# Kernel tuning notes

Measured on AMD Instinct MI355X. Metric: run time of the kernel, lower is better.

Reference implementation:

```python
import jax, jax.numpy as jnp
import numpy as np

SPAN_W = 8      # fixed span width (tokens per span)
HID = 150       # Score hidden dim (hardcoded in source)


def _score_mlp(x, w1, b1, w2, b2, w3, b3):
    # Linear->ReLU->(Dropout=id)->Linear->ReLU->(Dropout=id)->Linear ; out dim 1
    h = jax.nn.relu(x @ w1 + b1)
    h = jax.nn.relu(h @ w2 + b2)
    return h @ w3 + b3


def _make_mlp_params(key, in_dim):
    ks = jax.random.split(key, 6)
    s1 = 1.0 / np.sqrt(in_dim)
    s2 = 1.0 / np.sqrt(HID)
    return (
        jax.random.uniform(ks[0], (in_dim, HID), jnp.float32, -s1, s1),
        jax.random.uniform(ks[1], (HID,), jnp.float32, -s1, s1),
        jax.random.uniform(ks[2], (HID, HID), jnp.float32, -s2, s2),
        jax.random.uniform(ks[3], (HID,), jnp.float32, -s2, s2),
        jax.random.uniform(ks[4], (HID, 1), jnp.float32, -s2, s2),
        jax.random.uniform(ks[5], (1,), jnp.float32, -s2, s2),
    )


def setup_inputs() -> dict:
    key = jax.random.key(0)
    k_emb, k_sp, k_a, k_m, k_p = jax.random.split(key, 5)
    E = 768
    B, T, S = 2, 2048, 96
    encoded_docs = jax.random.normal(k_emb, (B, T, E), jnp.float32)
    span_starts = jnp.sort(
        jax.random.randint(k_sp, (B, S), 0, 2040, dtype=jnp.int64), axis=-1)
    aw1, ab1, aw2, ab2, aw3, ab3 = _make_mlp_params(k_a, E)          # attn Score
    mw1, mb1, mw2, mb2, mw3, mb3 = _make_mlp_params(k_m, 3 * E)      # mention Score
    pw1, pb1, pw2, pb2, pw3, pb3 = _make_mlp_params(k_p, 9 * E)      # pair Score
    return {
        "encoded_docs": encoded_docs, "span_starts": span_starts,
        "aw1": aw1, "ab1": ab1, "aw2": aw2, "ab2": ab2, "aw3": aw3, "ab3": ab3,
        "mw1": mw1, "mb1": mb1, "mw2": mw2, "mb2": mb2, "mw3": mw3, "mb3": mb3,
        "pw1": pw1, "pb1": pb1, "pw2": pw2, "pb2": pb2, "pw3": pw3, "pb3": pb3,
    }


def reference(encoded_docs, span_starts,
              aw1, ab1, aw2, ab2, aw3, ab3,
              mw1, mb1, mw2, mb2, mw3, mb3,
              pw1, pb1, pw2, pb2, pw3, pb3):
    B, T, E = encoded_docs.shape
    S = span_starts.shape[1]

    # --- MentionScore ---
    attns = _score_mlp(encoded_docs, aw1, ab1, aw2, ab2, aw3, ab3)  # [B,T,1]
    starts = span_starts                                              # [B,S]
    ends = starts + (SPAN_W - 1)
    g_start = jnp.take_along_axis(encoded_docs, starts[:, :, None], axis=1)  # [B,S,E]
    g_end = jnp.take_along_axis(encoded_docs, ends[:, :, None], axis=1)      # [B,S,E]
    tok_idx = starts[:, :, None] + jnp.arange(SPAN_W, dtype=starts.dtype)     # [B,S,W]
    flat = tok_idx.reshape(B, S * SPAN_W)
    span_emb = jnp.take_along_axis(encoded_docs, flat[:, :, None], axis=1).reshape(B, S, SPAN_W, E)
    span_attn = jnp.take_along_axis(attns, flat[:, :, None], axis=1).reshape(B, S, SPAN_W, 1)
    g_attn = jnp.sum(span_emb * span_attn, axis=2)                    # [B,S,E]
    g_i = jnp.concatenate([g_start, g_end, g_attn], axis=-1)          # [B,S,3E]
    mention_scores = _score_mlp(g_i, mw1, mb1, mw2, mb2, mw3, mb3)    # [B,S,1]

    # --- PairwiseScore: all pairs (i=span_1, j=span_2) ---
    gi = jnp.broadcast_to(g_i[:, :, None, :], (B, S, S, 3 * E))
    gj = jnp.broadcast_to(g_i[:, None, :, :], (B, S, S, 3 * E))
    pair = jnp.concatenate([gi, gj, gi * gj], axis=-1)                # [B,S,S,9E]
    pair_scores = _score_mlp(pair, pw1, pb1, pw2, pb2, pw3, pb3)      # [B,S,S,1]
    ext = (mention_scores[:, :, None, :] + mention_scores[:, None, :, :] + pair_scores) / 3.0
    return jnp.clip(ext, 0.0, 1.0)
```

## Files before the change

### kernel.cpp

```cpp
#include <hip/hip_runtime.h>

#define EDIM   768
#define E3     2304
#define HIDD   150
#define TT     2048
#define SS     96
#define BB     2

typedef unsigned short u16;
using frag   = __attribute__((ext_vector_type(8))) short;
using f32x4v = __attribute__((ext_vector_type(4))) float;
using u16x8  = __attribute__((ext_vector_type(8))) unsigned short;

__device__ __forceinline__ u16 bf16rn(float f) {
    union { float f; unsigned u; } v; v.f = f;
    unsigned r = v.u + 0x7FFF + ((v.u >> 16) & 1);
    return (u16)(r >> 16);
}
__device__ __forceinline__ float bf16tof(u16 h) {
    union { unsigned u; float f; } v; v.u = ((unsigned)h) << 16;
    return v.f;
}
__device__ __forceinline__ void split2(float f, u16& hi, u16& lo) {
    hi = bf16rn(f); lo = bf16rn(f - bf16tof(hi));
}
__device__ __forceinline__ int swzoff(int row, int qd) {
    return row * 32 + (((qd + (row >> 1)) & 3) << 3);
}
__device__ __forceinline__ void async16(const void* g, void* l) {
    __builtin_amdgcn_global_load_lds(
        (const __attribute__((address_space(1))) void*)g,
        (__attribute__((address_space(3))) void*)l, 16, 0, 0);
}

__global__ __launch_bounds__(256) void k_prep_all(
    const float* __restrict__ pw1, const float* __restrict__ mw1,
    const float* __restrict__ aw1, const float* __restrict__ aw2,
    const float* __restrict__ pw2, const float* __restrict__ mw2,
    u16* __restrict__ W12t_hi, u16* __restrict__ W12t_lo,
    u16* __restrict__ AW1t_hi, u16* __restrict__ AW1t_lo,
    u16* __restrict__ AW2t_hi, u16* __restrict__ AW2t_lo,
    u16* __restrict__ PW2t_hi, u16* __restrict__ PW2t_lo,
    u16* __restrict__ MW2t_hi, u16* __restrict__ MW2t_lo)
{
    __shared__ float tile[64][33];
    const int bi = blockIdx.x;
    const int t  = threadIdx.x;

    if (bi < 720) {
        const int k0 = (bi % 36) * 64;
        const int n0 = (bi / 36) * 32;
        const int seg = n0 / 160;
        const int nloc0 = n0 - seg * 160;
        for (int idx = t; idx < 2048; idx += 256) {
            const int kk = idx >> 5, nn = idx & 31;
            const int nl = nloc0 + nn;
            const int k  = k0 + kk;
            float v = 0.f;
            if (nl < HIDD) {
                if (seg == 0)      v = pw1[(long)k * HIDD + nl];
                else if (seg == 1) v = pw1[(long)(E3 + k) * HIDD + nl];
                else if (seg == 2) v = mw1[(long)k * HIDD + nl];
                else               v = pw1[(long)(2 * E3 + k) * HIDD + nl];
            }
            tile[kk][nn] = v;
        }
        __syncthreads();
        for (int idx = t; idx < 2048; idx += 256) {
            const int nn = idx >> 6, kk = idx & 63;
            u16 hi, lo; split2(tile[kk][nn], hi, lo);
            W12t_hi[(long)(n0 + nn) * E3 + k0 + kk] = hi;
            W12t_lo[(long)(n0 + nn) * E3 + k0 + kk] = lo;
        }
    } else if (bi < 1488) {
        const int k = bi - 720;
        if (t < 160) {
            float v = (t < HIDD) ? aw1[k * HIDD + t] : 0.f;
            u16 hi, lo; split2(v, hi, lo);
            AW1t_hi[(long)t * EDIM + k] = hi;
            AW1t_lo[(long)t * EDIM + k] = lo;
        }
    } else {
        const int r = bi - 1488;
        const int k = r % 160;
        const int which = r / 160;
        const float* src = (which == 0) ? aw2 : (which == 1) ? pw2 : mw2;
        u16* dh = (which == 0) ? AW2t_hi : (which == 1) ? PW2t_hi : MW2t_hi;
        u16* dl = (which == 0) ? AW2t_lo : (which == 1) ? PW2t_lo : MW2t_lo;
        if (t < 160) {
            float v = (t < HIDD && k < HIDD) ? src[k * HIDD + t] : 0.f;
            u16 hi, lo; split2(v, hi, lo);
            dh[t * 160 + k] = hi;
            dl[t * 160 + k] = lo;
        }
    }
}

__global__ __launch_bounds__(256) void k_attn1(
    const float* __restrict__ X, const int* __restrict__ spans,
    const u16* __restrict__ AW1t_hi, const u16* __restrict__ AW1t_lo,
    float* __restrict__ AH1)
{
    __shared__ __align__(16) u16 As_hi[32 * 40];
    __shared__ __align__(16) u16 As_lo[32 * 40];
    __shared__ __align__(16) u16 Bs_hi[160 * 40];
    __shared__ __align__(16) u16 Bs_lo[160 * 40];

    const int t    = threadIdx.x;
    const int lane = t & 63;
    const int m    = lane & 15;
    const int quad = lane >> 4;
    const int w    = t >> 6;
    const int mt   = (w & 1) * 16;
    const int nb   = (w >> 1) * 80;
    const int ks   = blockIdx.y;

    const int rr = t >> 3, q = t & 7;
    const int grow = blockIdx.x * 32 + rr;
    const int bs = grow >> 3, sw = grow & 7;
    const int b  = bs / SS;
    const int tok = spans[bs] + sw;
    const float* arow = X + ((long)b * TT + tok) * EDIM;

    f32x4v acc[5];
    #pragma unroll
    for (int ht = 0; ht < 5; ++ht)
        #pragma unroll
        for (int r = 0; r < 4; ++r) acc[ht][r] = 0.f;

    for (int tt = 0; tt < 6; ++tt) {
        const int kk0 = ks * 192 + tt * 32;
        {
            const float4 xv = *(const float4*)&arow[kk0 + q * 4];
            ushort4 hv, lv;
            split2(xv.x, hv.x, lv.x); split2(xv.y, hv.y, lv.y);
            split2(xv.z, hv.z, lv.z); split2(xv.w, hv.w, lv.w);
            *(ushort4*)&As_hi[rr * 40 + q * 4] = hv;
            *(ushort4*)&As_lo[rr * 40 + q * 4] = lv;
        }
        #pragma unroll
        for (int it = 0; it < 3; ++it) {
            const int v = t + it * 256;
            if (v < 640) {
                const int h = v >> 2, qq = v & 3;
                *(uint4*)&Bs_hi[h * 40 + qq * 8] = *(const uint4*)&AW1t_hi[(long)h * EDIM + kk0 + qq * 8];
                *(uint4*)&Bs_lo[h * 40 + qq * 8] = *(const uint4*)&AW1t_lo[(long)h * EDIM + kk0 + qq * 8];
            }
        }
        __syncthreads();
        const frag ah = *(const frag*)&As_hi[(mt + m) * 40 + quad * 8];
        const frag al = *(const frag*)&As_lo[(mt + m) * 40 + quad * 8];
        #pragma unroll
        for (int ht = 0; ht < 5; ++ht) {
            const frag bh = *(const frag*)&Bs_hi[(nb + ht * 16 + m) * 40 + quad * 8];
            const frag bl = *(const frag*)&Bs_lo[(nb + ht * 16 + m) * 40 + quad * 8];
            acc[ht] = __builtin_amdgcn_mfma_f32_16x16x32_bf16(al, bh, acc[ht], 0, 0, 0);
            acc[ht] = __builtin_amdgcn_mfma_f32_16x16x32_bf16(ah, bl, acc[ht], 0, 0, 0);
            acc[ht] = __builtin_amdgcn_mfma_f32_16x16x32_bf16(ah, bh, acc[ht], 0, 0, 0);
        }
        __syncthreads();
    }
    #pragma unroll
    for (int ht = 0; ht < 5; ++ht) {
        #pragma unroll
        for (int r = 0; r < 4; ++r) {
            const int row = blockIdx.x * 32 + mt + quad * 4 + r;
            const int col = nb + ht * 16 + m;
            if (col < HIDD) atomicAdd(&AH1[row * 160 + col], acc[ht][r]);
        }
    }
}

__global__ __launch_bounds__(256) void k_attn2(
    const float* __restrict__ AH1,
    const u16* __restrict__ AW2t_hi, const u16* __restrict__ AW2t_lo,
    const float* __restrict__ ab1, const float* __restrict__ ab2,
    const float* __restrict__ aw3, const float* __restrict__ ab3,
    float* __restrict__ attn_g)
{
    __shared__ __align__(16) u16 As_hi[32 * 40];
    __shared__ __align__(16) u16 As_lo[32 * 40];
    __shared__ __align__(16) u16 Bs_hi[160 * 40];
    __shared__ __align__(16) u16 Bs_lo[160 * 40];
    __shared__ float h1s[32 * 160];
    __shared__ float red[32];

    const int t    = threadIdx.x;
    const int lane = t & 63;
    const int m    = lane & 15;
    const int quad = lane >> 4;
    const int w    = t >> 6;
    const int mt   = (w & 1) * 16;
    const int nb   = (w >> 1) * 80;

    for (int u = t; u < 1280; u += 256) {
        const int row = u / 40, c4 = u - (u / 40) * 40;
        const int c0 = c4 * 4;
        const float4 v = *(const float4*)&AH1[(blockIdx.x * 32 + row) * 160 + c0];
        h1s[row * 160 + c0 + 0] = (c0 + 0 < HIDD) ? fmaxf(v.x + ab1[c0 + 0], 0.f) : 0.f;
        h1s[row * 160 + c0 + 1] = (c0 + 1 < HIDD) ? fmaxf(v.y + ab1[c0 + 1], 0.f) : 0.f;
        h1s[row * 160 + c0 + 2] = (c0 + 2 < HIDD) ? fmaxf(v.z + ab1[c0 + 2], 0.f) : 0.f;
        h1s[row * 160 + c0 + 3] = (c0 + 3 < HIDD) ? fmaxf(v.w + ab1[c0 + 3], 0.f) : 0.f;
    }
    if (t < 32) red[t] = 0.f;
    __syncthreads();

    const int rr = t >> 3, q = t & 7;
    f32x4v acc2[5];
    #pragma unroll
    for (int ht = 0; ht < 5; ++ht)
        #pragma unroll
        for (int r = 0; r < 4; ++r) acc2[ht][r] = 0.f;

    for (int kk = 0; kk < 5; ++kk) {
        {
            const float4 xv = *(const float4*)&h1s[rr * 160 + kk * 32 + q * 4];
            ushort4 hv, lv;
            split2(xv.x, hv.x, lv.x); split2(xv.y, hv.y, lv.y);
            split2(xv.z, hv.z, lv.z); split2(xv.w, hv.w, lv.w);
            *(ushort4*)&As_hi[rr * 40 + q * 4] = hv;
            *(ushort4*)&As_lo[rr * 40 + q * 4] = lv;
        }
        #pragma unroll
        for (int it = 0; it < 3; ++it) {
            const int v = t + it * 256;
            if (v < 640) {
                const int h = v >> 2, qq = v & 3;
                *(uint4*)&Bs_hi[h * 40 + qq * 8] = *(const uint4*)&AW2t_hi[h * 160 + kk * 32 + qq * 8];
                *(uint4*)&Bs_lo[h * 40 + qq * 8] = *(const uint4*)&AW2t_lo[h * 160 + kk * 32 + qq * 8];
            }
        }
        __syncthreads();
        const frag ah = *(const frag*)&As_hi[(mt + m) * 40 + quad * 8];
        const frag al = *(const frag*)&As_lo[(mt + m) * 40 + quad * 8];
        #pragma unroll
        for (int ht = 0; ht < 5; ++ht) {
            const frag bh = *(const frag*)&Bs_hi[(nb + ht * 16 + m) * 40 + quad * 8];
            const frag bl = *(const frag*)&Bs_lo[(nb + ht * 16 + m) * 40 + quad * 8];
            acc2[ht] = __builtin_amdgcn_mfma_f32_16x16x32_bf16(al, bh, acc2[ht], 0, 0, 0);
            acc2[ht] = __builtin_amdgcn_mfma_f32_16x16x32_bf16(ah, bl, acc2[ht], 0, 0, 0);
            acc2[ht] = __builtin_amdgcn_mfma_f32_16x16x32_bf16(ah, bh, acc2[ht], 0, 0, 0);
        }
        __syncthreads();
    }

    float s[4] = {0.f, 0.f, 0.f, 0.f};
    #pragma unroll
    for (int ht = 0; ht < 5; ++ht) {
        const int col = nb + ht * 16 + m;
        if (col < HIDD) {
            const float w3 = aw3[col];
            #pragma unroll
            for (int r = 0; r < 4; ++r)
                s[r] += fmaxf(acc2[ht][r] + ab2[col], 0.f) * w3;
        }
    }
    #pragma unroll
    for (int r = 0; r < 4; ++r) {
        for (int off = 8; off > 0; off >>= 1) s[r] += __shfl_down(s[r], off, 16);
    }
    if (m == 0) {
        #pragma unroll
        for (int r = 0; r < 4; ++r) atomicAdd(&red[mt + quad * 4 + r], s[r]);
    }
    __syncthreads();
    if (t < 32) attn_g[blockIdx.x * 32 + t] = red[t] + ab3[0];
}

__global__ __launch_bounds__(256) void k_span_g(
    const float* __restrict__ X, const int* __restrict__ spans,
    const float* __restrict__ attn_g, float* __restrict__ G_ws,
    u16* __restrict__ Gs_hi, u16* __restrict__ Gs_lo)
{
    __shared__ float a8[8];
    const int t  = threadIdx.x;
    const int bs = blockIdx.x;
    const int b  = bs / SS;
    const int start = spans[bs];
    const float* xb = X + ((long)b * TT + start) * EDIM;
    float* Gp = G_ws + (long)bs * E3;
    u16* Gh = Gs_hi + (long)bs * E3;
    u16* Gl = Gs_lo + (long)bs * E3;
    if (t < 8) a8[t] = attn_g[bs * 8 + t];
    __syncthreads();

    for (int e = t; e < EDIM; e += 256) {
        const float gs = xb[e];
        const float ge = xb[7 * EDIM + e];
        float ga = 0.f;
        #pragma unroll
        for (int w = 0; w < 8; ++w) ga += xb[w * EDIM + e] * a8[w];
        Gp[e] = gs; Gp[EDIM + e] = ge; Gp[2 * EDIM + e] = ga;
        u16 hi, lo;
        split2(gs, hi, lo); Gh[e] = hi;            Gl[e] = lo;
        split2(ge, hi, lo); Gh[EDIM + e] = hi;     Gl[EDIM + e] = lo;
        split2(ga, hi, lo); Gh[2 * EDIM + e] = hi; Gl[2 * EDIM + e] = lo;
    }
}

__global__ __launch_bounds__(256) void k_uvm(
    const u16* __restrict__ Gs_hi, const u16* __restrict__ Gs_lo,
    const u16* __restrict__ W9t_hi, const u16* __restrict__ W9t_lo,
    float* __restrict__ UVM)
{
    __shared__ __align__(16) u16 As_hi[64 * 40];
    __shared__ __align__(16) u16 As_lo[64 * 40];
    __shared__ __align__(16) u16 Bs_hi[160 * 40];
    __shared__ __align__(16) u16 Bs_lo[160 * 40];

    const int t    = threadIdx.x;
    const int mb   = blockIdx.x;
    const int nb   = blockIdx.y;
    const int ks   = blockIdx.z;
    const int lane = t & 63;
    const int m    = lane & 15;
    const int quad = lane >> 4;
    const int w    = t >> 6;
    const int mhalf = (w & 1) * 32;
    const int nbase = (w >> 1) * 80;
    const int arr = t >> 2, aq = t & 3;

    f32x4v acc[2][5];
    #pragma unroll
    for (int i = 0; i < 2; ++i)
        #pragma unroll
        for (int j = 0; j < 5; ++j)
            #pragma unroll
            for (int r = 0; r < 4; ++r) acc[i][j][r] = 0.f;

    for (int tt = 0; tt < 6; ++tt) {
        const int kk0 = ks * 192 + tt * 32;
        *(uint4*)&As_hi[arr * 40 + aq * 8] = *(const uint4*)&Gs_hi[(long)(mb * 64 + arr) * E3 + kk0 + aq * 8];
        *(uint4*)&As_lo[arr * 40 + aq * 8] = *(const uint4*)&Gs_lo[(long)(mb * 64 + arr) * E3 + kk0 + aq * 8];
        #pragma unroll
        for (int it = 0; it < 3; ++it) {
            const int v = t + it * 256;
            if (v < 640) {
                const int h = v >> 2, qq = v & 3;
                *(uint4*)&Bs_hi[h * 40 + qq * 8] = *(const uint4*)&W9t_hi[(long)(nb * 160 + h) * E3 + kk0 + qq * 8];
                *(uint4*)&Bs_lo[h * 40 + qq * 8] = *(const uint4*)&W9t_lo[(long)(nb * 160 + h) * E3 + kk0 + qq * 8];
            }
        }
        __syncthreads();
        frag ah[2], al[2];
        #pragma unroll
        for (int mt = 0; mt < 2; ++mt) {
            ah[mt] = *(const frag*)&As_hi[(mhalf + mt * 16 + m) * 40 + quad * 8];
            al[mt] = *(const frag*)&As_lo[(mhalf + mt * 16 + m) * 40 + quad * 8];
        }
        #pragma unroll
        for (int ht = 0; ht < 5; ++ht) {
            const frag bh = *(const frag*)&Bs_hi[(nbase + ht * 16 + m) * 40 + quad * 8];
            const frag bl = *(const frag*)&Bs_lo[(nbase + ht * 16 + m) * 40 + quad * 8];
            #pragma unroll
            for (int mt = 0; mt < 2; ++mt) {
                acc[mt][ht] = __builtin_amdgcn_mfma_f32_16x16x32_bf16(al[mt], bh, acc[mt][ht], 0, 0, 0);
                acc[mt][ht] = __builtin_amdgcn_mfma_f32_16x16x32_bf16(ah[mt], bl, acc[mt][ht], 0, 0, 0);
                acc[mt][ht] = __builtin_amdgcn_mfma_f32_16x16x32_bf16(ah[mt], bh, acc[mt][ht], 0, 0, 0);
            }
        }
        __syncthreads();
    }
    float* dst = UVM + (long)nb * (192 * 160);
    #pragma unroll
    for (int mt = 0; mt < 2; ++mt) {
        #pragma unroll
        for (int ht = 0; ht < 5; ++ht) {
            #pragma unroll
            for (int r = 0; r < 4; ++r) {
                const int row = mb * 64 + mhalf + mt * 16 + quad * 4 + r;
                const int c   = nbase + ht * 16 + m;
                atomicAdd(&dst[row * 160 + c], acc[mt][ht][r]);
            }
        }
    }
}

__global__ __launch_bounds__(256) void k_pairmm(
    const float* __restrict__ G_ws,
    const u16* __restrict__ PCt_hi, const u16* __restrict__ PCt_lo,
    float* __restrict__ H1parts)
{
    __shared__ float gis[768];
    __shared__ __align__(16) float gjst[96 * 32];
    __shared__ __align__(16) u16 As_hi[96 * 32];
    __shared__ __align__(16) u16 As_lo[96 * 32];
    __shared__ __align__(16) u16 Bs_hi[160 * 32];
    __shared__ __align__(16) u16 Bs_lo[160 * 32];

    const int t  = threadIdx.x;
    const int ks = blockIdx.x;
    const int i  = blockIdx.y;
    const int b  = blockIdx.z;
    const int ksbase = ks * 768;
    const int jt0 = i >> 4;
    const int ntiles = 6 - jt0;
    const int j0 = jt0 * 16;
    const int R  = 96 - j0;
    const int nI = R >> 3;

    const int lane = t & 63;
    const int m    = lane & 15;
    const int quad = lane >> 4;
    const int w    = t >> 6;
    const int hb   = (w & 1) * 80;
    const int apar = w >> 1;

    const int Bl_h  = lane >> 2;
    const int Bl_c  = lane & 3;
    const int gj_r  = lane >> 3;
    const int gj_c  = lane & 7;

    const float* Gi = G_ws + (long)(b * SS + i) * E3 + ksbase;
    for (int e = t; e < 768; e += 256) gis[e] = Gi[e];

    f32x4v acc[3][5];
    #pragma unroll
    for (int jt = 0; jt < 3; ++jt)
        #pragma unroll
        for (int ht = 0; ht < 5; ++ht)
            #pragma unroll
            for (int r = 0; r < 4; ++r) acc[jt][ht][r] = 0.f;

    for (int tt = 0; tt < 24; ++tt) {
        const int kk0 = ksbase + tt * 32;
        for (int q2 = w; q2 < 10; q2 += 4) {
            const int h  = q2 * 16 + Bl_h;
            const int qd = (Bl_c - (h >> 1)) & 3;
            const long so = (long)h * E3 + kk0 + qd * 8;
            async16(&PCt_hi[so], &Bs_hi[q2 * 512]);
            async16(&PCt_lo[so], &Bs_lo[q2 * 512]);
        }
        for (int g2 = w; g2 < nI; g2 += 4) {
            const int row = j0 + g2 * 8 + gj_r;
            async16(&G_ws[(long)(b * SS + row) * E3 + kk0 + gj_c * 4],
                    &gjst[g2 * 256]);
        }
        __syncthreads();

        for (int u = t; u < R * 4; u += 256) {
            const int rr = u >> 2, qd = u & 3;
            const float4 g0 = *(const float4*)&gjst[rr * 32 + qd * 8];
            const float4 g1 = *(const float4*)&gjst[rr * 32 + qd * 8 + 4];
            const int kl = tt * 32 + qd * 8;
            u16x8 hv, lv; u16 h, l;
            split2(g0.x * gis[kl + 0], h, l); hv[0] = h; lv[0] = l;
            split2(g0.y * gis[kl + 1], h, l); hv[1] = h; lv[1] = l;
            split2(g0.z * gis[kl + 2], h, l); hv[2] = h; lv[2] = l;
            split2(g0.w * gis[kl + 3], h, l); hv[3] = h; lv[3] = l;
            split2(g1.x * gis[kl + 4], h, l); hv[4] = h; lv[4] = l;
            split2(g1.y * gis[kl + 5], h, l); hv[5] = h; lv[5] = l;
            split2(g1.z * gis[kl + 6], h, l); hv[6] = h; lv[6] = l;
            split2(g1.w * gis[kl + 7], h, l); hv[7] = h; lv[7] = l;
            const int o = swzoff(rr, qd);
            *(u16x8*)&As_hi[o] = hv;
            *(u16x8*)&As_lo[o] = lv;
        }
        __syncthreads();

        frag ah[3], al[3];
        #pragma unroll
        for (int u = 0; u < 3; ++u) {
            const int a = apar + 2 * u;
            if (a < ntiles) {
                const int o = swzoff(a * 16 + m, quad);
                ah[u] = *(const frag*)&As_hi[o];
                al[u] = *(const frag*)&As_lo[o];
            }
        }
        #pragma unroll
        for (int ht = 0; ht < 5; ++ht) {
            const int o = swzoff(hb + ht * 16 + m, quad);
            const frag bh = *(const frag*)&Bs_hi[o];
            const frag bl = *(const frag*)&Bs_lo[o];
            #pragma unroll
            for (int u = 0; u < 3; ++u) {
                if (apar + 2 * u < ntiles) {
                    acc[u][ht] = __builtin_amdgcn_mfma_f32_16x16x32_bf16(al[u], bh, acc[u][ht], 0, 0, 0);
                    acc[u][ht] = __builtin_amdgcn_mfma_f32_16x16x32_bf16(ah[u], bl, acc[u][ht], 0, 0, 0);
                    acc[u][ht] = __builtin_amdgcn_mfma_f32_16x16x32_bf16(ah[u], bh, acc[u][ht], 0, 0, 0);
                }
            }
        }
        __syncthreads();
    }

    float* dst = H1parts + (long)ks * ((long)BB * SS * SS * 160);
    #pragma unroll
    for (int u = 0; u < 3; ++u) {
        const int a = apar + 2 * u;
        if (a < ntiles) {
            #pragma unroll
            for (int ht = 0; ht < 5; ++ht) {
                #pragma unroll
                for (int r = 0; r < 4; ++r) {
                    const int j = (jt0 + a) * 16 + quad * 4 + r;
                    const int h = hb + ht * 16 + m;
                    dst[((long)(b * SS + i) * SS + j) * 160 + h] = acc[u][ht][r];
                }
            }
        }
    }
}

__global__ __launch_bounds__(256) void k_pair2(
    const float* __restrict__ H1a, const float* __restrict__ H1b,
    const float* __restrict__ H1c,
    const float* __restrict__ U_ws, const float* __restrict__ V_ws,
    const float* __restrict__ pb1, const float* __restrict__ m_ws,
    const u16* __restrict__ PW2t_hi, const u16* __restrict__ PW2t_lo,
    const float* __restrict__ pb2, const float* __restrict__ pw3,
    const float* __restrict__ pb3,
    float* __restrict__ out)
{
    __shared__ __align__(16) u16 As_hi[96 * 168];
    __shared__ __align__(16) u16 As_lo[96 * 168];
    __shared__ __align__(16) u16 Bs_hi[160 * 40];
    __shared__ __align__(16) u16 Bs_lo[160 * 40];
    __shared__ float uv[160];
    __shared__ float red[96];

    const int t  = threadIdx.x;
    const int bi = blockIdx.x;
    const int b  = bi / SS;
    const int ii = bi - b * SS;

    if (t < 160) uv[t] = U_ws[bi * 160 + t] + ((t < HIDD) ? pb1[t] : 0.f);
    if (t < 96) red[t] = 0.f;
    __syncthreads();

    for (int u = t; u < 96 * 40; u += 256) {
        const int j = u / 40, hq = u - (u / 40) * 40;
        const int h0 = hq * 4;
        const int mn = ii < j ? ii : j;
        const int mx = ii < j ? j : ii;
        const long idx = (((long)b * SS + mn) * SS + mx) * 160 + h0;
        const float4 a  = *(const float4*)&H1a[idx];
        const float4 bb = *(const float4*)&H1b[idx];
        const float4 c  = *(const float4*)&H1c[idx];
        const float4 vv = *(const float4*)&V_ws[(b * SS + j) * 160 + h0];
        const float p0 = fmaxf(a.x + bb.x + c.x + vv.x + uv[h0 + 0], 0.f);
        const float p1 = fmaxf(a.y + bb.y + c.y + vv.y + uv[h0 + 1], 0.f);
        const float p2 = fmaxf(a.z + bb.z + c.z + vv.z + uv[h0 + 2], 0.f);
        const float p3 = fmaxf(a.w + bb.w + c.w + vv.w + uv[h0 + 3], 0.f);
        ushort4 hv, lv;
        split2(p0, hv.x, lv.x); split2(p1, hv.y, lv.y);
        split2(p2, hv.z, lv.z); split2(p3, hv.w, lv.w);
        *(ushort4*)&As_hi[j * 168 + h0] = hv;
        *(ushort4*)&As_lo[j * 168 + h0] = lv;
    }
    __syncthreads();

    const int lane = t & 63;
    const int m    = lane & 15;
    const int quad = lane >> 4;
    const int w    = t >> 6;
    const int jbs  = (w & 1) * 48;
    const int nbs  = (w >> 1) * 80;

    f32x4v acc[3][5];
    #pragma unroll
    for (int jt = 0; jt < 3; ++jt)
        #pragma unroll
        for (int ht = 0; ht < 5; ++ht)
            #pragma unroll
            for (int r = 0; r < 4; ++r) acc[jt][ht][r] = 0.f;

    for (int kk = 0; kk < 5; ++kk) {
        #pragma unroll
        for (int it = 0; it < 3; ++it) {
            const int v = t + it * 256;
            if (v < 640) {
                const int n = v >> 2, qq = v & 3;
                *(uint4*)&Bs_hi[n * 40 + qq * 8] = *(const uint4*)&PW2t_hi[n * 160 + kk * 32 + qq * 8];
                *(uint4*)&Bs_lo[n * 40 + qq * 8] = *(const uint4*)&PW2t_lo[n * 160 + kk * 32 + qq * 8];
            }
        }
        __syncthreads();
        frag ah[3], al[3];
        #pragma unroll
        for (int jt = 0; jt < 3; ++jt) {
            ah[jt] = *(const frag*)&As_hi[(jbs + jt * 16 + m) * 168 + kk * 32 + quad * 8];
            al[jt] = *(const frag*)&As_lo[(jbs + jt * 16 + m) * 168 + kk * 32 + quad * 8];
        }
        #pragma unroll
        for (int ht = 0; ht < 5; ++ht) {
            const frag bh = *(const frag*)&Bs_hi[(nbs + ht * 16 + m) * 40 + quad * 8];
            const frag bl = *(const frag*)&Bs_lo[(nbs + ht * 16 + m) * 40 + quad * 8];
            #pragma unroll
            for (int jt = 0; jt < 3; ++jt) {
                acc[jt][ht] = __builtin_amdgcn_mfma_f32_16x16x32_bf16(al[jt], bh, acc[jt][ht], 0, 0, 0);
                acc[jt][ht] = __builtin_amdgcn_mfma_f32_16x16x32_bf16(ah[jt], bl, acc[jt][ht], 0, 0, 0);
                acc[jt][ht] = __builtin_amdgcn_mfma_f32_16x16x32_bf16(ah[jt], bh, acc[jt][ht], 0, 0, 0);
            }
        }
        __syncthreads();
    }

    float s[3][4];
    #pragma unroll
    for (int jt = 0; jt < 3; ++jt)
        #pragma unroll
        for (int r = 0; r < 4; ++r) s[jt][r] = 0.f;
    #pragma unroll
    for (int ht = 0; ht < 5; ++ht) {
        const int col = nbs + ht * 16 + m;
        if (col < HIDD) {
            const float w3 = pw3[col];
            const float b2 = pb2[col];
            #pragma unroll
            for (int jt = 0; jt < 3; ++jt)
                #pragma unroll
                for (int r = 0; r < 4; ++r)
                    s[jt][r] += fmaxf(acc[jt][ht][r] + b2, 0.f) * w3;
        }
    }
    #pragma unroll
    for (int jt = 0; jt < 3; ++jt)
        #pragma unroll
        for (int r = 0; r < 4; ++r)
            for (int off = 8; off > 0; off >>= 1)
                s[jt][r] += __shfl_down(s[jt][r], off, 16);
    if (m == 0) {
        #pragma unroll
        for (int jt = 0; jt < 3; ++jt)
            #pragma unroll
            for (int r = 0; r < 4; ++r)
                atomicAdd(&red[jbs + jt * 16 + quad * 4 + r], s[jt][r]);
    }
    __syncthreads();

    if (t < 96) {
        const float sc = red[t] + pb3[0];
        const float v = (m_ws[bi] + m_ws[b * SS + t] + sc) * (1.f / 3.f);
        out[(long)bi * SS + t] = fminf(fmaxf(v, 0.f), 1.f);
    }
}

extern "C" void kernel_launch(void* const* d_in, const int* in_sizes, int n_in,
                              void* d_out, int out_size, void* d_ws, size_t ws_size,
                              hipStream_t stream)
{
    const float* X     = (const float*)d_in[0];
    const int*   spans = (const int*)  d_in[1];
    const float* aw1 = (const float*)d_in[2];
    const float* ab1 = (const float*)d_in[3];
    const float* aw2 = (const float*)d_in[4];
    const float* ab2 = (const float*)d_in[5];
    const float* aw3 = (const float*)d_in[6];
    const float* ab3 = (const float*)d_in[7];
    const float* mw1 = (const float*)d_in[8];
    const float* mb1 = (const float*)d_in[9];
    const float* mw2 = (const float*)d_in[10];
    const float* mb2 = (const float*)d_in[11];
    const float* mw3 = (const float*)d_in[12];
    const float* mb3 = (const float*)d_in[13];
    const float* pw1 = (const float*)d_in[14];
    const float* pb1 = (const float*)d_in[15];
    const float* pw2 = (const float*)d_in[16];
    const float* pb2 = (const float*)d_in[17];
    const float* pw3 = (const float*)d_in[18];
    const float* pb3 = (const float*)d_in[19];
    float* out = (float*)d_out;

    char* p = (char*)d_ws;
    float* attn_g  = (float*)p;  p += 6144;
    float* G_ws    = (float*)p;  p += (long)442368 * 4;
    u16*   Gs_hi   = (u16*)p;    p += (long)442368 * 2;
    u16*   Gs_lo   = (u16*)p;    p += (long)442368 * 2;
    float* UVM     = (float*)p;  p += (long)3 * 192 * 160 * 4;
    float* AH1     = (float*)p;  p += (long)1536 * 160 * 4;
    float* m_ws    = (float*)p;  p += 1024;
    u16*   W12t_hi = (u16*)p;    p += (long)640 * E3 * 2;
    u16*   W12t_lo = (u16*)p;    p += (long)640 * E3 * 2;
    u16*   AW1t_hi = (u16*)p;    p += (long)160 * EDIM * 2;
    u16*   AW1t_lo = (u16*)p;    p += (long)160 * EDIM * 2;
    u16*   AW2t_hi = (u16*)p;    p += 160 * 160 * 2;
    u16*   AW2t_lo = (u16*)p;    p += 160 * 160 * 2;
    u16*   PW2t_hi = (u16*)p;    p += 160 * 160 * 2;
    u16*   PW2t_lo = (u16*)p;    p += 160 * 160 * 2;
    u16*   MW2t_hi = (u16*)p;    p += 160 * 160 * 2;
    u16*   MW2t_lo = (u16*)p;    p += 160 * 160 * 2;
    float* H1parts = (float*)p;

    float* U_ws = UVM;
    float* V_ws = UVM + 192 * 160;
    float* M_ws = UVM + 2 * 192 * 160;
    const u16* PCt_hi = W12t_hi + (long)480 * E3;
    const u16* PCt_lo = W12t_lo + (long)480 * E3;

    hipMemsetAsync(UVM, 0, ((size_t)3 * 192 * 160 + (size_t)1536 * 160) * sizeof(float), stream);

    k_prep_all<<<dim3(1968), 256, 0, stream>>>(pw1, mw1, aw1, aw2, pw2, mw2,
                                               W12t_hi, W12t_lo, AW1t_hi, AW1t_lo,
                                               AW2t_hi, AW2t_lo, PW2t_hi, PW2t_lo,
                                               MW2t_hi, MW2t_lo);

    k_attn1<<<dim3(48, 4), 256, 0, stream>>>(X, spans, AW1t_hi, AW1t_lo, AH1);
    k_attn2<<<dim3(48), 256, 0, stream>>>(AH1, AW2t_hi, AW2t_lo, ab1, ab2, aw3, ab3, attn_g);
    k_span_g<<<dim3(BB * SS), 256, 0, stream>>>(X, spans, attn_g, G_ws, Gs_hi, Gs_lo);
    k_uvm<<<dim3(3, 3, 12), 256, 0, stream>>>(Gs_hi, Gs_lo, W12t_hi, W12t_lo, UVM);
    k_attn2<<<dim3(6), 256, 0, stream>>>(M_ws, MW2t_hi, MW2t_lo, mb1, mb2, mw3, mb3, m_ws);
    k_pairmm<<<dim3(3, SS, BB), 256, 0, stream>>>(G_ws, PCt_hi, PCt_lo, H1parts);

    const long H1sz = (long)BB * SS * SS * 160;
    k_pair2<<<dim3(BB * SS), 256, 0, stream>>>(
        H1parts, H1parts + H1sz, H1parts + 2 * H1sz,
        U_ws, V_ws, pb1, m_ws, PW2t_hi, PW2t_lo, pb2, pw3, pb3, out);
}
```

Baseline: 230.7 us.

## Merge uvm and pairmm into one heavy launch; split pair2 over column blocks

The UVM GEMM blocks and the pairwise first-layer GEMM blocks now run in a single launch of 684 blocks that branches on block id and shares one shared-memory buffer. Running both at once removes a kernel boundary and lets the small UVM blocks fill idle compute units while the pairmm blocks execute. The pair2 kernel is also split into three 32-column j-blocks per row, giving 576 blocks instead of 192 and lowering per-block shared memory. In exchange, the merged kernel has to reserve registers and shared memory for the larger of the two paths, and each pair2 block reloads the PW2 weight tiles.

```diff
diff --git a/kernel.cpp b/kernel.cpp
--- a/kernel.cpp
+++ b/kernel.cpp
@@ -298,205 +298,201 @@
     }
 }
 
-__global__ __launch_bounds__(256) void k_uvm(
+__global__ __launch_bounds__(256) void k_heavy(
+    const float* __restrict__ G_ws,
     const u16* __restrict__ Gs_hi, const u16* __restrict__ Gs_lo,
-    const u16* __restrict__ W9t_hi, const u16* __restrict__ W9t_lo,
-    float* __restrict__ UVM)
+    const u16* __restrict__ W12t_hi, const u16* __restrict__ W12t_lo,
+    const u16* __restrict__ PCt_hi, const u16* __restrict__ PCt_lo,
+    float* __restrict__ H1parts, float* __restrict__ UVM)
 {
-    __shared__ __align__(16) u16 As_hi[64 * 40];
-    __shared__ __align__(16) u16 As_lo[64 * 40];
-    __shared__ __align__(16) u16 Bs_hi[160 * 40];
-    __shared__ __align__(16) u16 Bs_lo[160 * 40];
-
-    const int t    = threadIdx.x;
-    const int mb   = blockIdx.x;
-    const int nb   = blockIdx.y;
-    const int ks   = blockIdx.z;
+    __shared__ __align__(16) char smem[48128];
+    const int id = blockIdx.x;
+    const int t  = threadIdx.x;
     const int lane = t & 63;
     const int m    = lane & 15;
     const int quad = lane >> 4;
     const int w    = t >> 6;
-    const int mhalf = (w & 1) * 32;
-    const int nbase = (w >> 1) * 80;
-    const int arr = t >> 2, aq = t & 3;
-
-    f32x4v acc[2][5];
-    #pragma unroll
-    for (int i = 0; i < 2; ++i)
-        #pragma unroll
-        for (int j = 0; j < 5; ++j)
-            #pragma unroll
-            for (int r = 0; r < 4; ++r) acc[i][j][r] = 0.f;
-
-    for (int tt = 0; tt < 6; ++tt) {
-        const int kk0 = ks * 192 + tt * 32;
-        *(uint4*)&As_hi[arr * 40 + aq * 8] = *(const uint4*)&Gs_hi[(long)(mb * 64 + arr) * E3 + kk0 + aq * 8];
-        *(uint4*)&As_lo[arr * 40 + aq * 8] = *(const uint4*)&Gs_lo[(long)(mb * 64 + arr) * E3 + kk0 + aq * 8];
-        #pragma unroll
-        for (int it = 0; it < 3; ++it) {
-            const int v = t + it * 256;
-            if (v < 640) {
-                const int h = v >> 2, qq = v & 3;
-                *(uint4*)&Bs_hi[h * 40 + qq * 8] = *(const uint4*)&W9t_hi[(long)(nb * 160 + h) * E3 + kk0 + qq * 8];
-                *(uint4*)&Bs_lo[h * 40 + qq * 8] = *(const uint4*)&W9t_lo[(long)(nb * 160 + h) * E3 + kk0 + qq * 8];
-            }
-        }
-        __syncthreads();
-        frag ah[2], al[2];
-        #pragma unroll
-        for (int mt = 0; mt < 2; ++mt) {
-            ah[mt] = *(const frag*)&As_hi[(mhalf + mt * 16 + m) * 40 + quad * 8];
-            al[mt] = *(const frag*)&As_lo[(mhalf + mt * 16 + m) * 40 + quad * 8];
-        }
-        #pragma unroll
-        for (int ht = 0; ht < 5; ++ht) {
-            const frag bh = *(const frag*)&Bs_hi[(nbase + ht * 16 + m) * 40 + quad * 8];
-            const frag bl = *(const frag*)&Bs_lo[(nbase + ht * 16 + m) * 40 + quad * 8];
-            #pragma unroll
-            for (int mt = 0; mt < 2; ++mt) {
-                acc[mt][ht] = __builtin_amdgcn_mfma_f32_16x16x32_bf16(al[mt], bh, acc[mt][ht], 0, 0, 0);
-                acc[mt][ht] = __builtin_amdgcn_mfma_f32_16x16x32_bf16(ah[mt], bl, acc[mt][ht], 0, 0, 0);
-                acc[mt][ht] = __builtin_amdgcn_mfma_f32_16x16x32_bf16(ah[mt], bh, acc[mt][ht], 0, 0, 0);
-            }
-        }
-        __syncthreads();
-    }
-    float* dst = UVM + (long)nb * (192 * 160);
-    #pragma unroll
-    for (int mt = 0; mt < 2; ++mt) {
-        #pragma unroll
-        for (int ht = 0; ht < 5; ++ht) {
-            #pragma unroll
-            for (int r = 0; r < 4; ++r) {
-                const int row = mb * 64 + mhalf + mt * 16 + quad * 4 + r;
-                const int c   = nbase + ht * 16 + m;
-                atomicAdd(&dst[row * 160 + c], acc[mt][ht][r]);
-            }
-        }
-    }
-}
-
-__global__ __launch_bounds__(256) void k_pairmm(
-    const float* __restrict__ G_ws,
-    const u16* __restrict__ PCt_hi, const u16* __restrict__ PCt_lo,
-    float* __restrict__ H1parts)
-{
-    __shared__ float gis[768];
-    __shared__ __align__(16) float gjst[96 * 32];
-    __shared__ __align__(16) u16 As_hi[96 * 32];
-    __shared__ __align__(16) u16 As_lo[96 * 32];
-    __shared__ __align__(16) u16 Bs_hi[160 * 32];
-    __shared__ __align__(16) u16 Bs_lo[160 * 32];
-
-    const int t  = threadIdx.x;
-    const int ks = blockIdx.x;
-    const int i  = blockIdx.y;
-    const int b  = blockIdx.z;
-    const int ksbase = ks * 768;
-    const int jt0 = i >> 4;
-    const int ntiles = 6 - jt0;
-    const int j0 = jt0 * 16;
-    const int R  = 96 - j0;
-    const int nI = R >> 3;
-
-    const int lane = t & 63;
-    const int m    = lane & 15;
-    const int quad = lane >> 4;
-    const int w    = t >> 6;
-    const int hb   = (w & 1) * 80;
-    const int apar = w >> 1;
-
-    const int Bl_h  = lane >> 2;
-    const int Bl_c  = lane & 3;
-    const int gj_r  = lane >> 3;
-    const int gj_c  = lane & 7;
-
-    const float* Gi = G_ws + (long)(b * SS + i) * E3 + ksbase;
-    for (int e = t; e < 768; e += 256) gis[e] = Gi[e];
-
-    f32x4v acc[3][5];
-    #pragma unroll
-    for (int jt = 0; jt < 3; ++jt)
-        #pragma unroll
-        for (int ht = 0; ht < 5; ++ht)
-            #pragma unroll
-            for (int r = 0; r < 4; ++r) acc[jt][ht][r] = 0.f;
-
-    for (int tt = 0; tt < 24; ++tt) {
-        const int kk0 = ksbase + tt * 32;
-        for (int q2 = w; q2 < 10; q2 += 4) {
-            const int h  = q2 * 16 + Bl_h;
-            const int qd = (Bl_c - (h >> 1)) & 3;
-            const long so = (long)h * E3 + kk0 + qd * 8;
-            async16(&PCt_hi[so], &Bs_hi[q2 * 512]);
-            async16(&PCt_lo[so], &Bs_lo[q2 * 512]);
-        }
-        for (int g2 = w; g2 < nI; g2 += 4) {
-            const int row = j0 + g2 * 8 + gj_r;
-            async16(&G_ws[(long)(b * SS + row) * E3 + kk0 + gj_c * 4],
-                    &gjst[g2 * 256]);
-        }
-        __syncthreads();
-
-        for (int u = t; u < R * 4; u += 256) {
-            const int rr = u >> 2, qd = u & 3;
-            const float4 g0 = *(const float4*)&gjst[rr * 32 + qd * 8];
-            const float4 g1 = *(const float4*)&gjst[rr * 32 + qd * 8 + 4];
-            const int kl = tt * 32 + qd * 8;
-            u16x8 hv, lv; u16 h, l;
-            split2(g0.x * gis[kl + 0], h, l); hv[0] = h; lv[0] = l;
-            split2(g0.y * gis[kl + 1], h, l); hv[1] = h; lv[1] = l;
-            split2(g0.z * gis[kl + 2], h, l); hv[2] = h; lv[2] = l;
-            split2(g0.w * gis[kl + 3], h, l); hv[3] = h; lv[3] = l;
-            split2(g1.x * gis[kl + 4], h, l); hv[4] = h; lv[4] = l;
-            split2(g1.y * gis[kl + 5], h, l); hv[5] = h; lv[5] = l;
-            split2(g1.z * gis[kl + 6], h, l); hv[6] = h; lv[6] = l;
-            split2(g1.w * gis[kl + 7], h, l); hv[7] = h; lv[7] = l;
-            const int o = swzoff(rr, qd);
-            *(u16x8*)&As_hi[o] = hv;
-            *(u16x8*)&As_lo[o] = lv;
-        }
-        __syncthreads();
-
-        frag ah[3], al[3];
+
+    if (id < 576) {
+        float* gis  = (float*)smem;
+        float* gjst = (float*)(smem + 3072);
+        u16* As_hi  = (u16*)(smem + 15360);
+        u16* As_lo  = (u16*)(smem + 21504);
+        u16* Bs_hi  = (u16*)(smem + 27648);
+        u16* Bs_lo  = (u16*)(smem + 37888);
+
+        const int ks = id % 3;
+        const int i  = (id / 3) % SS;
+        const int b  = id / 288;
+        const int ksbase = ks * 768;
+        const int jt0 = i >> 4;
+        const int ntiles = 6 - jt0;
+        const int j0 = jt0 * 16;
+        const int R  = 96 - j0;
+        const int nI = R >> 3;
+
+        const int hb   = (w & 1) * 80;
+        const int apar = w >> 1;
+        const int Bl_h = lane >> 2;
+        const int Bl_c = lane & 3;
+        const int gj_r = lane >> 3;
+        const int gj_c = lane & 7;
+
+        const float* Gi = G_ws + (long)(b * SS + i) * E3 + ksbase;
+        for (int e = t; e < 768; e += 256) gis[e] = Gi[e];
+
+        f32x4v acc[3][5];
+        #pragma unroll
+        for (int jt = 0; jt < 3; ++jt)
+            #pragma unroll
+            for (int ht = 0; ht < 5; ++ht)
+                #pragma unroll
+                for (int r = 0; r < 4; ++r) acc[jt][ht][r] = 0.f;
+
+        for (int tt = 0; tt < 24; ++tt) {
+            const int kk0 = ksbase + tt * 32;
+            for (int q2 = w; q2 < 10; q2 += 4) {
+                const int h  = q2 * 16 + Bl_h;
+                const int qd = (Bl_c - (h >> 1)) & 3;
+                const long so = (long)h * E3 + kk0 + qd * 8;
+                async16(&PCt_hi[so], &Bs_hi[q2 * 512]);
+                async16(&PCt_lo[so], &Bs_lo[q2 * 512]);
+            }
+            for (int g2 = w; g2 < nI; g2 += 4) {
+                const int row = j0 + g2 * 8 + gj_r;
+                async16(&G_ws[(long)(b * SS + row) * E3 + kk0 + gj_c * 4],
+                        &gjst[g2 * 256]);
+            }
+            __syncthreads();
+
+            for (int u = t; u < R * 4; u += 256) {
+                const int rr = u >> 2, qd = u & 3;
+                const float4 g0 = *(const float4*)&gjst[rr * 32 + qd * 8];
+                const float4 g1 = *(const float4*)&gjst[rr * 32 + qd * 8 + 4];
+                const int kl = tt * 32 + qd * 8;
+                u16x8 hv, lv; u16 h, l;
+                split2(g0.x * gis[kl + 0], h, l); hv[0] = h; lv[0] = l;
+                split2(g0.y * gis[kl + 1], h, l); hv[1] = h; lv[1] = l;
+                split2(g0.z * gis[kl + 2], h, l); hv[2] = h; lv[2] = l;
+                split2(g0.w * gis[kl + 3], h, l); hv[3] = h; lv[3] = l;
+                split2(g1.x * gis[kl + 4], h, l); hv[4] = h; lv[4] = l;
+                split2(g1.y * gis[kl + 5], h, l); hv[5] = h; lv[5] = l;
+                split2(g1.z * gis[kl + 6], h, l); hv[6] = h; lv[6] = l;
+                split2(g1.w * gis[kl + 7], h, l); hv[7] = h; lv[7] = l;
+                const int o = swzoff(rr, qd);
+                *(u16x8*)&As_hi[o] = hv;
+                *(u16x8*)&As_lo[o] = lv;
+            }
+            __syncthreads();
+
+            frag ah[3], al[3];
+            #pragma unroll
+            for (int u = 0; u < 3; ++u) {
+                const int a = apar + 2 * u;
+                if (a < ntiles) {
+                    const int o = swzoff(a * 16 + m, quad);
+                    ah[u] = *(const frag*)&As_hi[o];
+                    al[u] = *(const frag*)&As_lo[o];
+                }
+            }
+            #pragma unroll
+            for (int ht = 0; ht < 5; ++ht) {
+                const int o = swzoff(hb + ht * 16 + m, quad);
+                const frag bh = *(const frag*)&Bs_hi[o];
+                const frag bl = *(const frag*)&Bs_lo[o];
+                #pragma unroll
+                for (int u = 0; u < 3; ++u) {
+                    if (apar + 2 * u < ntiles) {
+                        acc[u][ht] = __builtin_amdgcn_mfma_f32_16x16x32_bf16(al[u], bh, acc[u][ht], 0, 0, 0);
+                        acc[u][ht] = __builtin_amdgcn_mfma_f32_16x16x32_bf16(ah[u], bl, acc[u][ht], 0, 0, 0);
+                        acc[u][ht] = __builtin_amdgcn_mfma_f32_16x16x32_bf16(ah[u], bh, acc[u][ht], 0, 0, 0);
+                    }
+                }
+            }
+            __syncthreads();
+        }
+
+        float* dst = H1parts + (long)ks * ((long)BB * SS * SS * 160);
         #pragma unroll
         for (int u = 0; u < 3; ++u) {
             const int a = apar + 2 * u;
             if (a < ntiles) {
-                const int o = swzoff(a * 16 + m, quad);
-                ah[u] = *(const frag*)&As_hi[o];
-                al[u] = *(const frag*)&As_lo[o];
-            }
-        }
-        #pragma unroll
-        for (int ht = 0; ht < 5; ++ht) {
-            const int o = swzoff(hb + ht * 16 + m, quad);
-            const frag bh = *(const frag*)&Bs_hi[o];
-            const frag bl = *(const frag*)&Bs_lo[o];
-            #pragma unroll
-            for (int u = 0; u < 3; ++u) {
-                if (apar + 2 * u < ntiles) {
-                    acc[u][ht] = __builtin_amdgcn_mfma_f32_16x16x32_bf16(al[u], bh, acc[u][ht], 0, 0, 0);
-                    acc[u][ht] = __builtin_amdgcn_mfma_f32_16x16x32_bf16(ah[u], bl, acc[u][ht], 0, 0, 0);
-                    acc[u][ht] = __builtin_amdgcn_mfma_f32_16x16x32_bf16(ah[u], bh, acc[u][ht], 0, 0, 0);
+                #pragma unroll
+                for (int ht = 0; ht < 5; ++ht) {
+                    #pragma unroll
+                    for (int r = 0; r < 4; ++r) {
+                        const int j = (jt0 + a) * 16 + quad * 4 + r;
+                        const int h = hb + ht * 16 + m;
+                        dst[((long)(b * SS + i) * SS + j) * 160 + h] = acc[u][ht][r];
+                    }
                 }
             }
         }
-        __syncthreads();
-    }
-
-    float* dst = H1parts + (long)ks * ((long)BB * SS * SS * 160);
-    #pragma unroll
-    for (int u = 0; u < 3; ++u) {
-        const int a = apar + 2 * u;
-        if (a < ntiles) {
+    } else {
+        u16* As_hi = (u16*)smem;
+        u16* As_lo = (u16*)(smem + 5120);
+        u16* Bs_hi = (u16*)(smem + 10240);
+        u16* Bs_lo = (u16*)(smem + 23040);
+
+        const int u0 = id - 576;
+        const int mb = u0 % 3;
+        const int nb = (u0 / 3) % 3;
+        const int kz = u0 / 9;
+        const int mhalf = (w & 1) * 32;
+        const int nbase = (w >> 1) * 80;
+        const int arr = t >> 2, aq = t & 3;
+
+        f32x4v acc[2][5];
+        #pragma unroll
+        for (int i = 0; i < 2; ++i)
+            #pragma unroll
+            for (int j = 0; j < 5; ++j)
+                #pragma unroll
+                for (int r = 0; r < 4; ++r) acc[i][j][r] = 0.f;
+
+        for (int tt = 0; tt < 6; ++tt) {
+            const int kk0 = kz * 192 + tt * 32;
+            *(uint4*)&As_hi[arr * 40 + aq * 8] = *(const uint4*)&Gs_hi[(long)(mb * 64 + arr) * E3 + kk0 + aq * 8];
+            *(uint4*)&As_lo[arr * 40 + aq * 8] = *(const uint4*)&Gs_lo[(long)(mb * 64 + arr) * E3 + kk0 + aq * 8];
+            #pragma unroll
+            for (int it = 0; it < 3; ++it) {
+                const int v = t + it * 256;
+                if (v < 640) {
+                    const int h = v >> 2, qq = v & 3;
+                    *(uint4*)&Bs_hi[h * 40 + qq * 8] = *(const uint4*)&W12t_hi[(long)(nb * 160 + h) * E3 + kk0 + qq * 8];
+                    *(uint4*)&Bs_lo[h * 40 + qq * 8] = *(const uint4*)&W12t_lo[(long)(nb * 160 + h) * E3 + kk0 + qq * 8];
+                }
+            }
+            __syncthreads();
+            frag ah[2], al[2];
+            #pragma unroll
+            for (int mt = 0; mt < 2; ++mt) {
+                ah[mt] = *(const frag*)&As_hi[(mhalf + mt * 16 + m) * 40 + quad * 8];
+                al[mt] = *(const frag*)&As_lo[(mhalf + mt * 16 + m) * 40 + quad * 8];
+            }
+            #pragma unroll
+            for (int ht = 0; ht < 5; ++ht) {
+                const frag bh = *(const frag*)&Bs_hi[(nbase + ht * 16 + m) * 40 + quad * 8];
+                const frag bl = *(const frag*)&Bs_lo[(nbase + ht * 16 + m) * 40 + quad * 8];
+                #pragma unroll
+                for (int mt = 0; mt < 2; ++mt) {
+                    acc[mt][ht] = __builtin_amdgcn_mfma_f32_16x16x32_bf16(al[mt], bh, acc[mt][ht], 0, 0, 0);
+                    acc[mt][ht] = __builtin_amdgcn_mfma_f32_16x16x32_bf16(ah[mt], bl, acc[mt][ht], 0, 0, 0);
+                    acc[mt][ht] = __builtin_amdgcn_mfma_f32_16x16x32_bf16(ah[mt], bh, acc[mt][ht], 0, 0, 0);
+                }
+            }
+            __syncthreads();
+        }
+        float* dst = UVM + (long)nb * (192 * 160);
+        #pragma unroll
+        for (int mt = 0; mt < 2; ++mt) {
             #pragma unroll
             for (int ht = 0; ht < 5; ++ht) {
                 #pragma unroll
                 for (int r = 0; r < 4; ++r) {
-                    const int j = (jt0 + a) * 16 + quad * 4 + r;
-                    const int h = hb + ht * 16 + m;
-                    dst[((long)(b * SS + i) * SS + j) * 160 + h] = acc[u][ht][r];
+                    const int row = mb * 64 + mhalf + mt * 16 + quad * 4 + r;
+                    const int c   = nbase + ht * 16 + m;
+                    atomicAdd(&dst[row * 160 + c], acc[mt][ht][r]);
                 }
             }
         }
@@ -504,8 +500,7 @@
 }
 
 __global__ __launch_bounds__(256) void k_pair2(
-    const float* __restrict__ H1a, const float* __restrict__ H1b,
-    const float* __restrict__ H1c,
+    const float* __restrict__ H1parts,
     const float* __restrict__ U_ws, const float* __restrict__ V_ws,
     const float* __restrict__ pb1, const float* __restrict__ m_ws,
     const u16* __restrict__ PW2t_hi, const u16* __restrict__ PW2t_lo,
@@ -513,41 +508,45 @@
     const float* __restrict__ pb3,
     float* __restrict__ out)
 {
-    __shared__ __align__(16) u16 As_hi[96 * 168];
-    __shared__ __align__(16) u16 As_lo[96 * 168];
+    __shared__ __align__(16) u16 As_hi[32 * 168];
+    __shared__ __align__(16) u16 As_lo[32 * 168];
     __shared__ __align__(16) u16 Bs_hi[160 * 40];
     __shared__ __align__(16) u16 Bs_lo[160 * 40];
     __shared__ float uv[160];
-    __shared__ float red[96];
-
+    __shared__ float red[32];
+
+    const long partsz = (long)BB * SS * SS * 160;
     const int t  = threadIdx.x;
-    const int bi = blockIdx.x;
+    const int js = blockIdx.x;
+    const int bi = blockIdx.y;
     const int b  = bi / SS;
     const int ii = bi - b * SS;
+    const int jb0 = js * 32;
 
     if (t < 160) uv[t] = U_ws[bi * 160 + t] + ((t < HIDD) ? pb1[t] : 0.f);
-    if (t < 96) red[t] = 0.f;
+    if (t < 32) red[t] = 0.f;
     __syncthreads();
 
-    for (int u = t; u < 96 * 40; u += 256) {
-        const int j = u / 40, hq = u - (u / 40) * 40;
+    for (int u = t; u < 32 * 40; u += 256) {
+        const int jl = u / 40, hq = u - (u / 40) * 40;
+        const int j  = jb0 + jl;
         const int h0 = hq * 4;
         const int mn = ii < j ? ii : j;
         const int mx = ii < j ? j : ii;
         const long idx = (((long)b * SS + mn) * SS + mx) * 160 + h0;
-        const float4 a  = *(const float4*)&H1a[idx];
-        const float4 bb = *(const float4*)&H1b[idx];
-        const float4 c  = *(const float4*)&H1c[idx];
         const float4 vv = *(const float4*)&V_ws[(b * SS + j) * 160 + h0];
-        const float p0 = fmaxf(a.x + bb.x + c.x + vv.x + uv[h0 + 0], 0.f);
-        const float p1 = fmaxf(a.y + bb.y + c.y + vv.y + uv[h0 + 1], 0.f);
-        const float p2 = fmaxf(a.z + bb.z + c.z + vv.z + uv[h0 + 2], 0.f);
-        const float p3 = fmaxf(a.w + bb.w + c.w + vv.w + uv[h0 + 3], 0.f);
+        const float4 a0 = *(const float4*)&H1parts[idx];
+        const float4 a1 = *(const float4*)&H1parts[partsz + idx];
+        const float4 a2 = *(const float4*)&H1parts[2 * partsz + idx];
+        const float p0 = fmaxf(a0.x + a1.x + a2.x + vv.x + uv[h0 + 0], 0.f);
+        const float p1 = fmaxf(a0.y + a1.y + a2.y + vv.y + uv[h0 + 1], 0.f);
+        const float p2 = fmaxf(a0.z + a1.z + a2.z + vv.z + uv[h0 + 2], 0.f);
+        const float p3 = fmaxf(a0.w + a1.w + a2.w + vv.w + uv[h0 + 3], 0.f);
         ushort4 hv, lv;
         split2(p0, hv.x, lv.x); split2(p1, hv.y, lv.y);
         split2(p2, hv.z, lv.z); split2(p3, hv.w, lv.w);
-        *(ushort4*)&As_hi[j * 168 + h0] = hv;
-        *(ushort4*)&As_lo[j * 168 + h0] = lv;
+        *(ushort4*)&As_hi[jl * 168 + h0] = hv;
+        *(ushort4*)&As_lo[jl * 168 + h0] = lv;
     }
     __syncthreads();
 
@@ -555,16 +554,14 @@
     const int m    = lane & 15;
     const int quad = lane >> 4;
     const int w    = t >> 6;
-    const int jbs  = (w & 1) * 48;
-    const int nbs  = (w >> 1) * 80;
-
-    f32x4v acc[3][5];
-    #pragma unroll
-    for (int jt = 0; jt < 3; ++jt)
-        #pragma unroll
-        for (int ht = 0; ht < 5; ++ht)
-            #pragma unroll
-            for (int r = 0; r < 4; ++r) acc[jt][ht][r] = 0.f;
+    const int jt   = w >> 1;
+    const int nbs  = (w & 1) * 80;
+
+    f32x4v acc[5];
+    #pragma unroll
+    for (int ht = 0; ht < 5; ++ht)
+        #pragma unroll
+        for (int r = 0; r < 4; ++r) acc[ht][r] = 0.f;
 
     for (int kk = 0; kk < 5; ++kk) {
         #pragma unroll
@@ -577,31 +574,20 @@
             }
         }
         __syncthreads();
-        frag ah[3], al[3];
-        #pragma unroll
-        for (int jt = 0; jt < 3; ++jt) {
-            ah[jt] = *(const frag*)&As_hi[(jbs + jt * 16 + m) * 168 + kk * 32 + quad * 8];
-            al[jt] = *(const frag*)&As_lo[(jbs + jt * 16 + m) * 168 + kk * 32 + quad * 8];
-        }
+        const frag ah = *(const frag*)&As_hi[(jt * 16 + m) * 168 + kk * 32 + quad * 8];
+        const frag al = *(const frag*)&As_lo[(jt * 16 + m) * 168 + kk * 32 + quad * 8];
         #pragma unroll
         for (int ht = 0; ht < 5; ++ht) {
             const frag bh = *(const frag*)&Bs_hi[(nbs + ht * 16 + m) * 40 + quad * 8];
             const frag bl = *(const frag*)&Bs_lo[(nbs + ht * 16 + m) * 40 + quad * 8];
-            #pragma unroll
-            for (int jt = 0; jt < 3; ++jt) {
-                acc[jt][ht] = __builtin_amdgcn_mfma_f32_16x16x32_bf16(al[jt], bh, acc[jt][ht], 0, 0, 0);
-                acc[jt][ht] = __builtin_amdgcn_mfma_f32_16x16x32_bf16(ah[jt], bl, acc[jt][ht], 0, 0, 0);
-                acc[jt][ht] = __builtin_amdgcn_mfma_f32_16x16x32_bf16(ah[jt], bh, acc[jt][ht], 0, 0, 0);
-            }
+            acc[ht] = __builtin_amdgcn_mfma_f32_16x16x32_bf16(al, bh, acc[ht], 0, 0, 0);
+            acc[ht] = __builtin_amdgcn_mfma_f32_16x16x32_bf16(ah, bl, acc[ht], 0, 0, 0);
+            acc[ht] = __builtin_amdgcn_mfma_f32_16x16x32_bf16(ah, bh, acc[ht], 0, 0, 0);
         }
         __syncthreads();
     }
 
-    float s[3][4];
-    #pragma unroll
-    for (int jt = 0; jt < 3; ++jt)
-        #pragma unroll
-        for (int r = 0; r < 4; ++r) s[jt][r] = 0.f;
+    float s[4] = {0.f, 0.f, 0.f, 0.f};
     #pragma unroll
     for (int ht = 0; ht < 5; ++ht) {
         const int col = nbs + ht * 16 + m;
@@ -609,31 +595,26 @@
             const float w3 = pw3[col];
             const float b2 = pb2[col];
             #pragma unroll
-            for (int jt = 0; jt < 3; ++jt)
-                #pragma unroll
-                for (int r = 0; r < 4; ++r)
-                    s[jt][r] += fmaxf(acc[jt][ht][r] + b2, 0.f) * w3;
-        }
-    }
-    #pragma unroll
-    for (int jt = 0; jt < 3; ++jt)
+            for (int r = 0; r < 4; ++r)
+                s[r] += fmaxf(acc[ht][r] + b2, 0.f) * w3;
+        }
+    }
+    #pragma unroll
+    for (int r = 0; r < 4; ++r)
+        for (int off = 8; off > 0; off >>= 1)
+            s[r] += __shfl_down(s[r], off, 16);
+    if (m == 0) {
         #pragma unroll
         for (int r = 0; r < 4; ++r)
-            for (int off = 8; off > 0; off >>= 1)
-                s[jt][r] += __shfl_down(s[jt][r], off, 16);
-    if (m == 0) {
-        #pragma unroll
-        for (int jt = 0; jt < 3; ++jt)
-            #pragma unroll
-            for (int r = 0; r < 4; ++r)
-                atomicAdd(&red[jbs + jt * 16 + quad * 4 + r], s[jt][r]);
+            atomicAdd(&red[jt * 16 + quad * 4 + r], s[r]);
     }
     __syncthreads();
 
-    if (t < 96) {
+    if (t < 32) {
+        const int j = jb0 + t;
         const float sc = red[t] + pb3[0];
-        const float v = (m_ws[bi] + m_ws[b * SS + t] + sc) * (1.f / 3.f);
-        out[(long)bi * SS + t] = fminf(fmaxf(v, 0.f), 1.f);
+        const float v = (m_ws[bi] + m_ws[b * SS + j] + sc) * (1.f / 3.f);
+        out[(long)bi * SS + j] = fminf(fmaxf(v, 0.f), 1.f);
     }
 }
 
@@ -699,12 +680,12 @@
     k_attn1<<<dim3(48, 4), 256, 0, stream>>>(X, spans, AW1t_hi, AW1t_lo, AH1);
     k_attn2<<<dim3(48), 256, 0, stream>>>(AH1, AW2t_hi, AW2t_lo, ab1, ab2, aw3, ab3, attn_g);
     k_span_g<<<dim3(BB * SS), 256, 0, stream>>>(X, spans, attn_g, G_ws, Gs_hi, Gs_lo);
-    k_uvm<<<dim3(3, 3, 12), 256, 0, stream>>>(Gs_hi, Gs_lo, W12t_hi, W12t_lo, UVM);
+
+    k_heavy<<<dim3(684), 256, 0, stream>>>(G_ws, Gs_hi, Gs_lo, W12t_hi, W12t_lo,
+                                           PCt_hi, PCt_lo, H1parts, UVM);
+
     k_attn2<<<dim3(6), 256, 0, stream>>>(M_ws, MW2t_hi, MW2t_lo, mb1, mb2, mw3, mb3, m_ws);
-    k_pairmm<<<dim3(3, SS, BB), 256, 0, stream>>>(G_ws, PCt_hi, PCt_lo, H1parts);
-
-    const long H1sz = (long)BB * SS * SS * 160;
-    k_pair2<<<dim3(BB * SS), 256, 0, stream>>>(
-        H1parts, H1parts + H1sz, H1parts + 2 * H1sz,
-        U_ws, V_ws, pb1, m_ws, PW2t_hi, PW2t_lo, pb2, pw3, pb3, out);
-}
+
+    k_pair2<<<dim3(3, BB * SS), 256, 0, stream>>>(
+        H1parts, U_ws, V_ws, pb1, m_ws, PW2t_hi, PW2t_lo, pb2, pw3, pb3, out);
+}
```

Measured after the change: 215.6 us. -6.6%, faster.
